# Optimization experiments

Measured on AMD Instinct MI355X. Metric: run time of the kernel, lower is better.

Reference implementation:

```python
import jax, jax.numpy as jnp
import numpy as np

B, N = 2, 2048
DIM, NH, DH = 640, 10, 64
DINNER = 2560
L = 4
DEMB = 32
NTOKS = [128, 64]
NFEAT = 19
FDIM = 280
FEATD = DIM - DEMB * len(NTOKS)  # 576
SQRTD = float(np.sqrt(DH))


def _ln(x, g, b, eps=1e-5):
    m = jnp.mean(x, -1, keepdims=True)
    v = jnp.var(x, -1, keepdims=True)
    return (x - m) * jax.lax.rsqrt(v + eps) * g + b


def setup_inputs() -> dict:
    key = jax.random.key(0)
    ks = iter(jax.random.split(key, 32))
    s = 0.05
    return {
        "x_feats": jax.random.normal(next(ks), (B, N, NFEAT), jnp.float32),
        "x_toks": jax.random.randint(next(ks), (B, N, 2), 0, 64),
        "mask": jnp.ones((B, N), jnp.float32),
        "emb0": jax.random.normal(next(ks), (NTOKS[0] + 1, DEMB)) * s,
        "emb1": jax.random.normal(next(ks), (NTOKS[1] + 1, DEMB)) * s,
        "feat_w": jax.random.normal(next(ks), (FEATD, NFEAT)) * s,
        "feat_b": jnp.zeros((FEATD,)),
        "qkv_w": jax.random.normal(next(ks), (L, 3 * DIM, DIM)) * s,
        "qkv_b": jnp.zeros((L, 3 * DIM)),
        "o_w": jax.random.normal(next(ks), (L, DIM, DIM)) * s,
        "ln1_g": jnp.ones((L, DIM)), "ln1_b": jnp.zeros((L, DIM)),
        "ln2_g": jnp.ones((L, DIM)), "ln2_b": jnp.zeros((L, DIM)),
        "p1_w": jax.random.normal(next(ks), (L, DINNER, DIM)) * s,
        "p1_b": jnp.zeros((L, DINNER)),
        "p2_w": jax.random.normal(next(ks), (L, DIM, DINNER)) * s,
        "p2_b": jnp.zeros((L, DIM)),
        "fn_g": jnp.ones((DIM,)), "fn_b": jnp.zeros((DIM,)),
        "lin1_w": jax.random.normal(next(ks), (FDIM, DIM)) * s,
        "lin1_b": jnp.zeros((FDIM,)),
        "rb1_w": jax.random.normal(next(ks), (FDIM, FDIM)) * s,
        "rb1_b": jnp.zeros((FDIM,)),
        "rb2_w": jax.random.normal(next(ks), (FDIM, FDIM)) * s,
        "rb2_b": jnp.zeros((FDIM,)),
        "out_w": jax.random.normal(next(ks), (1, FDIM)) * s,
        "out_b": jnp.zeros((1,)),
    }


def _forward(x_feats, x_toks, mask, emb0, emb1, feat_w, feat_b,
             qkv_w, qkv_b, o_w, ln1_g, ln1_b, ln2_g, ln2_b,
             p1_w, p1_b, p2_w, p2_b, fn_g, fn_b,
             lin1_w, lin1_b, rb1_w, rb1_b, rb2_w, rb2_b, out_w, out_b):
    # mask outer product [B,N,N]; additive mask 0 where allowed, -1e20 elsewhere
    mask2 = jnp.einsum('bi,bj->bij', mask, mask)
    add_mask = jnp.where(mask2 > 0, 0.0, -1e20)

    # embeddings + feature projection -> [B,N,DIM]
    Z = jnp.concatenate([emb0[x_toks[..., 0]], emb1[x_toks[..., 1]],
                         x_feats @ feat_w.T + feat_b], axis=-1)

    def layer(Z, prm):
        qw, qb, ow, g1, b1, g2, b2, w1, c1, w2, c2 = prm
        inp = Z
        Zn = _ln(Z, g1, b1)
        # qkv reshaped to [B,N,H,3*DH], chunked along last dim: V, Q, K
        qkv = (Zn @ qw.T + qb).reshape(B, N, NH, 3 * DH)
        V, Q, K = qkv[..., :DH], qkv[..., DH:2 * DH], qkv[..., 2 * DH:]
        W = jnp.einsum('bnhd,bmhd->bhnm', Q, K) / SQRTD + add_mask[:, None]
        W = jax.nn.softmax(W, axis=3) * mask2[:, None]  # post-softmax mult mask
        attn = jnp.einsum('bhnm,bmhd->bnhd', W, V).reshape(B, N, DIM)
        Z = jax.nn.leaky_relu(attn) @ ow.T + inp  # leaky_relu BEFORE o_net
        inp = Z
        Zn = _ln(Z, g2, b2)
        Z = jax.nn.relu(Zn @ w1.T + c1) @ w2.T + c2 + inp
        return Z, None

    Z, _ = jax.lax.scan(layer, Z,
                        (qkv_w, qkv_b, o_w, ln1_g, ln1_b, ln2_g, ln2_b,
                         p1_w, p1_b, p2_w, p2_b))
    Z = _ln(Z, fn_g, fn_b)
    # ranking head: 1x1 convs == per-token linears
    h = Z @ lin1_w.T + lin1_b
    h = h + (jax.nn.relu(h @ rb1_w.T + rb1_b) @ rb2_w.T + rb2_b)
    return (h @ out_w.T + out_b)[..., 0]  # [B,N]


def reference(x_feats, x_toks, mask, emb0, emb1, feat_w, feat_b,
              qkv_w, qkv_b, o_w, ln1_g, ln1_b, ln2_g, ln2_b,
              p1_w, p1_b, p2_w, p2_b, fn_g, fn_b,
              lin1_w, lin1_b, rb1_w, rb1_b, rb2_w, rb2_b, out_w, out_b):
    return _forward(x_feats, x_toks, mask, emb0, emb1, feat_w, feat_b,
                    qkv_w, qkv_b, o_w, ln1_g, ln1_b, ln2_g, ln2_b,
                    p1_w, p1_b, p2_w, p2_b, fn_g, fn_b,
                    lin1_w, lin1_b, rb1_w, rb1_b, rb2_w, rb2_b, out_w, out_b)
```

## Files before the change

kernel.cpp:

```cpp
#include <hip/hip_runtime.h>

#define B_ 2
#define N_ 2048
#define DIM_ 640
#define NH_ 10
#define DH_ 64
#define DINNER_ 2560
#define L_ 4
#define FDIM_ 280
#define FDIMP_ 320
#define FEATD_ 576
#define NFEAT_ 19
#define ROWS_ (B_*N_)
#define NSPLIT_ 4
#define NT2_ 16

typedef __attribute__((ext_vector_type(8))) unsigned short ushort8;
typedef __attribute__((ext_vector_type(4))) unsigned short ushort4v;
typedef __attribute__((ext_vector_type(4))) unsigned int u32x4;
typedef __attribute__((ext_vector_type(8))) __bf16 bf16x8;
typedef __attribute__((ext_vector_type(4))) __bf16 bf16x4;
typedef __attribute__((ext_vector_type(4))) float f32x4;
typedef __attribute__((ext_vector_type(2))) unsigned int u32x2;

static __device__ __forceinline__ unsigned short f2bf(float f){
  unsigned int u = __builtin_bit_cast(unsigned int, f);
  u += 0x7fffu + ((u >> 16) & 1u);
  return (unsigned short)(u >> 16);
}

static __device__ __forceinline__ void cvt4(const float* __restrict__ s, unsigned short* __restrict__ d){
  f32x4 v = *(const f32x4*)s;
  ushort4v r;
  r[0]=f2bf(v[0]); r[1]=f2bf(v[1]); r[2]=f2bf(v[2]); r[3]=f2bf(v[3]);
  *(ushort4v*)d = r;
}

static __device__ __forceinline__ f32x4 mfma16(ushort8 a, ushort8 b, f32x4 c){
  return __builtin_amdgcn_mfma_f32_16x16x32_bf16(
      __builtin_bit_cast(bf16x8, a), __builtin_bit_cast(bf16x8, b), c, 0, 0, 0);
}

#define GLD(src,dst) __builtin_amdgcn_global_load_lds((const __attribute__((address_space(1))) void*)(src), (__attribute__((address_space(3))) void*)(dst), 16, 0, 0)

#define SEG0 4915200
#define SEG1 1638400
#define SEG2 6553600
#define SEG3 6553600
#define SEG4 179200
#define SEG5 89600
#define SEG6 89600
#define SEG7 655360
#define SEG8 655360
#define SEG9 4096
#define E0 SEG0
#define E9 (SEG0+SEG1+SEG2+SEG3+SEG4+SEG5+SEG6+SEG7+SEG8+SEG9)

__global__ __launch_bounds__(256) void prep_kernel(
    const float* __restrict__ qkv_w, const float* __restrict__ o_w,
    const float* __restrict__ p1_w, const float* __restrict__ p2_w,
    const float* __restrict__ lin1_w, const float* __restrict__ rb1_w,
    const float* __restrict__ rb2_w, const float* __restrict__ mask,
    unsigned short* __restrict__ qkvw, unsigned short* __restrict__ oww,
    unsigned short* __restrict__ p1w, unsigned short* __restrict__ p2w,
    unsigned short* __restrict__ l1w, unsigned short* __restrict__ r1w,
    unsigned short* __restrict__ r2w, unsigned int* __restrict__ hb1z,
    unsigned int* __restrict__ hb2z, float* __restrict__ mbb)
{
  for (int i = blockIdx.x*256 + threadIdx.x; i < E9/4; i += gridDim.x*256){
    int j = i*4;
    if (j < E0) { cvt4(qkv_w+j, qkvw+j); continue; }
    j -= E0;
    if (j < SEG1) { cvt4(o_w+j, oww+j); continue; }
    j -= SEG1;
    if (j < SEG2) { cvt4(p1_w+j, p1w+j); continue; }
    j -= SEG2;
    if (j < SEG3) { cvt4(p2_w+j, p2w+j); continue; }
    j -= SEG3;
    if (j < SEG4) { cvt4(lin1_w+j, l1w+j); continue; }
    j -= SEG4;
    if (j < SEG5) {
      #pragma unroll
      for (int e=0;e<4;e++){ int jj=j+e; int r=jj/FDIMP_, c=jj-r*FDIMP_;
        r1w[jj] = (c<FDIM_) ? f2bf(rb1_w[r*FDIM_+c]) : (unsigned short)0; }
      continue; }
    j -= SEG5;
    if (j < SEG6) {
      #pragma unroll
      for (int e=0;e<4;e++){ int jj=j+e; int r=jj/FDIMP_, c=jj-r*FDIMP_;
        r2w[jj] = (c<FDIM_) ? f2bf(rb2_w[r*FDIM_+c]) : (unsigned short)0; }
      continue; }
    j -= SEG6;
    if (j < SEG7) { *(u32x4*)(hb1z+j) = u32x4{0u,0u,0u,0u}; continue; }
    j -= SEG7;
    if (j < SEG8) { *(u32x4*)(hb2z+j) = u32x4{0u,0u,0u,0u}; continue; }
    j -= SEG8;
    {
      f32x4 m = *(const f32x4*)(mask+j);
      f32x4 r;
      #pragma unroll
      for (int e=0;e<4;e++) r[e] = (m[e] > 0.f) ? 0.f : -1e30f;
      *(f32x4*)(mbb+j) = r;
    }
  }
}

__global__ __launch_bounds__(256) void embed_kernel(const float* __restrict__ xf,
    const int* __restrict__ xt, const float* __restrict__ e0, const float* __restrict__ e1,
    const float* __restrict__ fw, const float* __restrict__ fb, float* __restrict__ Z){
  int row = blockIdx.x;
  __shared__ float f[NFEAT_];
  int t = threadIdx.x;
  if (t < NFEAT_) f[t] = xf[row*NFEAT_ + t];
  __syncthreads();
  if (t < 32) {
    int tok0 = xt[row*2];
    Z[(size_t)row*DIM_ + t] = e0[tok0*32 + t];
  } else if (t < 64) {
    int tok1 = xt[row*2+1];
    Z[(size_t)row*DIM_ + t] = e1[tok1*32 + (t-32)];
  }
  for (int fo = t; fo < FEATD_; fo += 256){
    float acc = fb[fo];
    #pragma unroll
    for (int k=0;k<NFEAT_;k++) acc += f[k]*fw[fo*NFEAT_+k];
    Z[(size_t)row*DIM_ + 64 + fo] = acc;
  }
}

__global__ __launch_bounds__(256) void ln_kernel(const float* __restrict__ X,
    const float* __restrict__ g, const float* __restrict__ bb,
    unsigned short* __restrict__ out){
  int lane = threadIdx.x & 63;
  int row = blockIdx.x*4 + (threadIdx.x >> 6);
  const float* x = X + (size_t)row*DIM_;
  float v[10]; float s=0.f, sq=0.f;
  #pragma unroll
  for (int j=0;j<10;j++){ float t = x[lane + j*64]; v[j]=t; s+=t; sq+=t*t; }
  #pragma unroll
  for (int off=1; off<64; off<<=1){ s += __shfl_xor(s, off, 64); sq += __shfl_xor(sq, off, 64); }
  float mean = s*(1.f/DIM_);
  float var = sq*(1.f/DIM_) - mean*mean;
  float rstd = rsqrtf(var + 1e-5f);
  unsigned short* o = out + (size_t)row*DIM_;
  #pragma unroll
  for (int j=0;j<10;j++){ int c = lane + j*64; o[c] = f2bf((v[j]-mean)*rstd*g[c] + bb[c]); }
}

template<bool BIAS, bool RELU, bool RES, bool OUTF, bool OUTB>
__global__ __launch_bounds__(256) void gemm_kernel(
    const unsigned short* __restrict__ A, int lda,
    const unsigned short* __restrict__ Bw, int ldb,
    const float* __restrict__ bias,
    const float* __restrict__ Res, int ldres,
    float* __restrict__ Cf, int ldcf,
    unsigned short* __restrict__ Cb, int ldcb,
    int Ncols, int K)
{
  __shared__ __align__(128) unsigned short As[2][8192];
  __shared__ __align__(128) unsigned short Bs[2][8192];
  int t = threadIdx.x;
  int wid = t >> 6, lane = t & 63;
  int wr = wid >> 1, wc = wid & 1;
  int lg = lane >> 4, lm = lane & 15;
  int orig = blockIdx.y*gridDim.x + blockIdx.x;
  int nwg = gridDim.x*gridDim.y;
  int wg = ((orig & 7) * (nwg >> 3)) + (orig >> 3);
  int bx = wg % gridDim.x, by = wg / gridDim.x;
  int row0 = by * 128;
  int col0 = bx * 128;

  const unsigned short* aSrc[4];
  const unsigned short* bSrc[4];
  #pragma unroll
  for (int j=0;j<4;j++){
    int s = t + j*256;
    int r = s >> 3;
    int c = (s & 7) ^ (((r >> 2) & 1) << 1);
    aSrc[j] = A + (size_t)(row0 + r)*lda + c*8;
    int br = col0 + r; if (br >= Ncols) br = Ncols - 1;
    bSrc[j] = Bw + (size_t)br*ldb + c*8;
  }

  f32x4 acc[4][4];
  #pragma unroll
  for (int m=0;m<4;m++)
    #pragma unroll
    for (int n=0;n<4;n++) acc[m][n] = f32x4{0.f,0.f,0.f,0.f};

  int nk = K >> 6;
  #pragma unroll
  for (int j=0;j<4;j++){
    GLD(aSrc[j], &As[0][(t + j*256)*8]);
    GLD(bSrc[j], &Bs[0][(t + j*256)*8]);
  }

  int swz = (lm & 4) >> 1;
  for (int tk=0; tk<nk; ++tk){
    int cur = tk & 1;
    if (tk+1 < nk){
      int kt = (tk+1) << 6;
      #pragma unroll
      for (int j=0;j<4;j++){
        GLD(aSrc[j]+kt, &As[cur^1][(t + j*256)*8]);
        GLD(bSrc[j]+kt, &Bs[cur^1][(t + j*256)*8]);
      }
      asm volatile("s_waitcnt vmcnt(8)" ::: "memory");
    } else {
      asm volatile("s_waitcnt vmcnt(0)" ::: "memory");
    }
    __builtin_amdgcn_s_barrier();
    asm volatile("" ::: "memory");
    const unsigned short* Ac = &As[cur][0];
    const unsigned short* Bc = &Bs[cur][0];
    #pragma unroll
    for (int kk=0;kk<2;kk++){
      int ch = ((kk*4 + lg) ^ swz) * 8;
      ushort8 af[4], bfr[4];
      #pragma unroll
      for (int m=0;m<4;m++) af[m] = *(const ushort8*)(Ac + (wr*64 + m*16 + lm)*64 + ch);
      #pragma unroll
      for (int n=0;n<4;n++) bfr[n] = *(const ushort8*)(Bc + (wc*64 + n*16 + lm)*64 + ch);
      #pragma unroll
      for (int m=0;m<4;m++)
        #pragma unroll
        for (int n=0;n<4;n++)
          acc[m][n] = mfma16(af[m], bfr[n], acc[m][n]);
    }
    asm volatile("" ::: "memory");
    __builtin_amdgcn_s_barrier();
  }

  #pragma unroll
  for (int m=0;m<4;m++){
    int rbase = row0 + wr*64 + m*16 + lg*4;
    #pragma unroll
    for (int n=0;n<4;n++){
      int cc = col0 + wc*64 + n*16 + lm;
      if (cc < Ncols){
        float bv = 0.f;
        if (BIAS) bv = bias[cc];
        #pragma unroll
        for (int rr=0;rr<4;rr++){
          float v = acc[m][n][rr] + bv;
          if (RELU) v = fmaxf(v, 0.f);
          if (RES) v += Res[(size_t)(rbase+rr)*ldres + cc];
          if (OUTF) Cf[(size_t)(rbase+rr)*ldcf + cc] = v;
          if (OUTB) Cb[(size_t)(rbase+rr)*ldcb + cc] = f2bf(v);
        }
      }
    }
  }
}

template<bool BIAS, bool RELU, bool RES, bool OUTF, bool OUTB>
__global__ __launch_bounds__(256) void gemm64_kernel(
    const unsigned short* __restrict__ A, int lda,
    const unsigned short* __restrict__ Bw, int ldb,
    const float* __restrict__ bias,
    const float* __restrict__ Res, int ldres,
    float* __restrict__ Cf, int ldcf,
    unsigned short* __restrict__ Cb, int ldcb,
    int Ncols, int K)
{
  __shared__ __align__(128) unsigned short As[2][64*64];
  __shared__ __align__(128) unsigned short Bs[2][64*64];
  int t = threadIdx.x;
  int wid = t >> 6, lane = t & 63;
  int wr = wid >> 1, wc = wid & 1;
  int lg = lane >> 4, lm = lane & 15;
  int orig = blockIdx.y*gridDim.x + blockIdx.x;
  int nwg = gridDim.x*gridDim.y;
  int wg = ((orig & 7) * (nwg >> 3)) + (orig >> 3);
  int bx = wg % gridDim.x, by = wg / gridDim.x;
  int row0 = by * 64;
  int col0 = bx * 64;

  int ar0 = t >> 3;
  int ar1 = ar0 + 32;
  int aq = (t & 7) ^ (((ar0 >> 2) & 1) << 1);
  const unsigned short* a0 = A + (size_t)(row0+ar0)*lda + aq*8;
  const unsigned short* a1 = A + (size_t)(row0+ar1)*lda + aq*8;
  int br0 = col0+ar0; if (br0 >= Ncols) br0 = Ncols-1;
  int br1 = col0+ar1; if (br1 >= Ncols) br1 = Ncols-1;
  const unsigned short* b0 = Bw + (size_t)br0*ldb + aq*8;
  const unsigned short* b1 = Bw + (size_t)br1*ldb + aq*8;
  int l0 = t*8, l1 = (t+256)*8;

  f32x4 acc[2][2];
  #pragma unroll
  for (int m=0;m<2;m++)
    #pragma unroll
    for (int n=0;n<2;n++) acc[m][n] = f32x4{0.f,0.f,0.f,0.f};

  int nk = K >> 6;
  GLD(a0, &As[0][l0]); GLD(b0, &Bs[0][l0]);
  GLD(a1, &As[0][l1]); GLD(b1, &Bs[0][l1]);

  int swz = (lm & 4) >> 1;
  for (int tk=0; tk<nk; ++tk){
    int cur = tk & 1;
    if (tk+1 < nk){
      int koff = (tk+1) << 6;
      GLD(a0+koff, &As[cur^1][l0]); GLD(b0+koff, &Bs[cur^1][l0]);
      GLD(a1+koff, &As[cur^1][l1]); GLD(b1+koff, &Bs[cur^1][l1]);
      asm volatile("s_waitcnt vmcnt(4)" ::: "memory");
    } else {
      asm volatile("s_waitcnt vmcnt(0)" ::: "memory");
    }
    __builtin_amdgcn_s_barrier();
    asm volatile("" ::: "memory");
    const unsigned short* Ac = &As[cur][0];
    const unsigned short* Bc = &Bs[cur][0];
    #pragma unroll
    for (int kk=0;kk<2;kk++){
      int ch = ((kk*4 + lg) ^ swz) * 8;
      ushort8 af[2], bfr[2];
      #pragma unroll
      for (int m=0;m<2;m++) af[m] = *(const ushort8*)(Ac + (wr*32 + m*16 + lm)*64 + ch);
      #pragma unroll
      for (int n=0;n<2;n++) bfr[n] = *(const ushort8*)(Bc + (wc*32 + n*16 + lm)*64 + ch);
      #pragma unroll
      for (int m=0;m<2;m++)
        #pragma unroll
        for (int n=0;n<2;n++)
          acc[m][n] = mfma16(af[m], bfr[n], acc[m][n]);
    }
    asm volatile("" ::: "memory");
    __builtin_amdgcn_s_barrier();
  }

  #pragma unroll
  for (int m=0;m<2;m++){
    int rbase = row0 + wr*32 + m*16 + lg*4;
    #pragma unroll
    for (int n=0;n<2;n++){
      int cc = col0 + wc*32 + n*16 + lm;
      if (cc < Ncols){
        float bv = 0.f;
        if (BIAS) bv = bias[cc];
        #pragma unroll
        for (int rr=0;rr<4;rr++){
          float v = acc[m][n][rr] + bv;
          if (RELU) v = fmaxf(v, 0.f);
          if (RES) v += Res[(size_t)(rbase+rr)*ldres + cc];
          if (OUTF) Cf[(size_t)(rbase+rr)*ldcf + cc] = v;
          if (OUTB) Cb[(size_t)(rbase+rr)*ldcb + cc] = f2bf(v);
        }
      }
    }
  }
}

__global__ __launch_bounds__(256) void attn_kernel(const unsigned short* __restrict__ qkv,
    const float* __restrict__ mb, unsigned short* __restrict__ op, float* __restrict__ lpp){
  int bh = blockIdx.y; int b = bh/NH_, h = bh%NH_;
  int t = threadIdx.x; int wid = t>>6, lane = t&63, lg = lane>>4, lm = lane&15;
  int q0 = blockIdx.x*64 + wid*16;
  int k0 = blockIdx.z * (NT2_*32);
  size_t prow = (size_t)blockIdx.z*ROWS_ + b*N_;

  __shared__ __align__(128) unsigned short Ks[2][2048];
  __shared__ __align__(128) unsigned short Vs[2][2048];
  __shared__ __align__(16) float maskL[NT2_*32];

  const size_t base = (size_t)b*N_*1920 + (size_t)h*192;
  const size_t kvoff = (size_t)k0*1920;

  int kk0 = t>>3, kc0 = (t&7)^(kk0&7);
  const unsigned short* kS0 = qkv + base + kvoff + 128 + (size_t)kk0*1920 + kc0*8;
  int vk0 = ((t>>5)<<2)|((t>>1)&3), vd0 = (((t>>3)&3)<<1)|(t&1);
  const unsigned short* vS0 = qkv + base + kvoff + (size_t)vk0*1920 + vd0*8;

  ushort8 qf[2];
  #pragma unroll
  for (int ss=0; ss<2; ss++)
    qf[ss] = *(const ushort8*)(qkv + base + (size_t)(q0+lm)*1920 + 64 + ss*32 + lg*8);
  float cb2 = mb[b*N_ + q0 + lm] - 17.3123405f;

  if (t < 128) GLD(mb + b*N_ + k0 + t*4, &maskL[t*4]);
  GLD(kS0, &Ks[0][t*8]);
  GLD(vS0, &Vs[0][t*8]);

  float lp = 0.f;
  f32x4 o[4];
  #pragma unroll
  for (int dn=0;dn<4;dn++) o[dn] = f32x4{0.f,0.f,0.f,0.f};

  for (int ii=0; ii<NT2_; ++ii){
    int cur = ii & 1;
    if (ii < NT2_ - 1){
      const size_t adv = (size_t)(ii+1)*32*1920;
      GLD(kS0+adv, &Ks[1-cur][t*8]);
      GLD(vS0+adv, &Vs[1-cur][t*8]);
      asm volatile("s_waitcnt vmcnt(2)" ::: "memory");
    } else {
      asm volatile("s_waitcnt vmcnt(0)" ::: "memory");
    }
    __builtin_amdgcn_s_barrier();
    asm volatile("" ::: "memory");

    const unsigned short* Kc = &Ks[cur][0];
    f32x4 sf[2];
    #pragma unroll
    for (int c=0;c<2;c++){
      int krow = c*16 + lm;
      f32x4 s = f32x4{0.f,0.f,0.f,0.f};
      #pragma unroll
      for (int ss=0;ss<2;ss++){
        ushort8 kf = *(const ushort8*)(Kc + (krow*8 + ((ss*4+lg)^(krow&7)))*8);
        s = mfma16(kf, qf[ss], s);
      }
      sf[c] = s;
    }
    f32x4 mkv[2];
    #pragma unroll
    for (int c=0;c<2;c++) mkv[c] = *(const f32x4*)&maskL[ii*32 + c*16 + lg*4];

    unsigned vsb = (unsigned)(size_t)(__attribute__((address_space(3))) unsigned short*)&Vs[cur][0];
    unsigned a0 = vsb + lg*512 + lm*8;
    u32x2 vb[2][4];
    asm volatile(
      "ds_read_b64_tr_b16 %0, %4 offset:0\n\t"
      "ds_read_b64_tr_b16 %1, %4 offset:128\n\t"
      "ds_read_b64_tr_b16 %2, %4 offset:256\n\t"
      "ds_read_b64_tr_b16 %3, %4 offset:384"
      : "=&v"(vb[0][0]),"=&v"(vb[0][1]),"=&v"(vb[0][2]),"=&v"(vb[0][3]) : "v"(a0));
    asm volatile(
      "ds_read_b64_tr_b16 %0, %4 offset:2048\n\t"
      "ds_read_b64_tr_b16 %1, %4 offset:2176\n\t"
      "ds_read_b64_tr_b16 %2, %4 offset:2304\n\t"
      "ds_read_b64_tr_b16 %3, %4 offset:2432"
      : "=&v"(vb[1][0]),"=&v"(vb[1][1]),"=&v"(vb[1][2]),"=&v"(vb[1][3]) : "v"(a0));

    float pm[2][4]; bf16x4 pa[2];
    #pragma unroll
    for (int c=0;c<2;c++){
      #pragma unroll
      for (int r=0;r<4;r++){
        float x = fmaf(sf[c][r], 0.18033688f, cb2 + mkv[c][r]);
        pm[c][r] = __builtin_amdgcn_exp2f(x);
      }
      lp += (pm[c][0]+pm[c][1]) + (pm[c][2]+pm[c][3]);
      pa[c] = bf16x4{(__bf16)pm[c][0], (__bf16)pm[c][1], (__bf16)pm[c][2], (__bf16)pm[c][3]};
    }

#define PVM(dn_, c_) asm("v_mfma_f32_16x16x16_bf16 %0, %1, %2, %0" \
      : "+v"(o[dn_]) : "v"(__builtin_bit_cast(u32x2, pa[c_])), "v"(vb[c_][dn_]))
    asm volatile("s_waitcnt lgkmcnt(4)" ::: "memory");
    __builtin_amdgcn_sched_barrier(0);
    __builtin_amdgcn_s_setprio(1);
    PVM(0,0); PVM(1,0); PVM(2,0); PVM(3,0);
    asm volatile("s_waitcnt lgkmcnt(0)" ::: "memory");
    __builtin_amdgcn_sched_barrier(0);
    PVM(0,1); PVM(1,1); PVM(2,1); PVM(3,1);
    __builtin_amdgcn_s_setprio(0);
#undef PVM
    asm volatile("" ::: "memory");
    __builtin_amdgcn_s_barrier();
  }

  float s = lp;
  s += __shfl_xor(s, 16, 64);
  s += __shfl_xor(s, 32, 64);
  if (lg == 0) lpp[(prow + q0 + lm)*NH_ + h] = s;
  #pragma unroll
  for (int r=0;r<4;r++){
    unsigned short* ob = op + (prow + q0 + lg*4 + r)*DIM_ + h*64;
    #pragma unroll
    for (int dn=0;dn<4;dn++)
      ob[dn*16 + lm] = f2bf(o[dn][r]);
  }
}

__global__ __launch_bounds__(256) void attnred_kernel(const unsigned short* __restrict__ op,
    const float* __restrict__ lpp, unsigned short* __restrict__ att){
  int idx = blockIdx.x*256 + threadIdx.x;
  int row = idx / 80;
  int c8 = (idx - row*80) * 8;
  int h = c8 >> 6;
  float l = 0.f;
  #pragma unroll
  for (int s=0;s<NSPLIT_;s++) l += lpp[((size_t)s*ROWS_ + row)*NH_ + h];
  float inv = 1.0f / fmaxf(l, 1e-30f);
  float acc[8] = {0.f,0.f,0.f,0.f,0.f,0.f,0.f,0.f};
  #pragma unroll
  for (int s=0;s<NSPLIT_;s++){
    ushort8 v = *(const ushort8*)(op + ((size_t)s*ROWS_ + row)*DIM_ + c8);
    #pragma unroll
    for (int j=0;j<8;j++) acc[j] += __builtin_bit_cast(float, (unsigned)v[j] << 16);
  }
  ushort8 rr;
  #pragma unroll
  for (int j=0;j<8;j++){
    float v = acc[j] * inv;
    v = (v >= 0.f) ? v : 0.01f*v;
    rr[j] = f2bf(v);
  }
  *(ushort8*)(att + (size_t)row*DIM_ + c8) = rr;
}

__global__ __launch_bounds__(256) void out_kernel(const float* __restrict__ hf,
    const float* __restrict__ ow, const float* __restrict__ ob, float* __restrict__ out){
  int lane = threadIdx.x & 63;
  int row = blockIdx.x*4 + (threadIdx.x>>6);
  const float* x = hf + (size_t)row*FDIM_;
  float s = 0.f;
  for (int j=lane;j<FDIM_;j+=64) s += x[j]*ow[j];
  #pragma unroll
  for (int off=1; off<64; off<<=1) s += __shfl_xor(s, off, 64);
  if (lane==0) out[row] = s + ob[0];
}

extern "C" void kernel_launch(void* const* d_in, const int* in_sizes, int n_in,
                              void* d_out, int out_size, void* d_ws, size_t ws_size,
                              hipStream_t stream)
{
  const float* x_feats = (const float*)d_in[0];
  const int*   x_toks  = (const int*)d_in[1];
  const float* mask    = (const float*)d_in[2];
  const float* emb0    = (const float*)d_in[3];
  const float* emb1    = (const float*)d_in[4];
  const float* feat_w  = (const float*)d_in[5];
  const float* feat_b  = (const float*)d_in[6];
  const float* qkv_w   = (const float*)d_in[7];
  const float* qkv_b   = (const float*)d_in[8];
  const float* o_w     = (const float*)d_in[9];
  const float* ln1_g   = (const float*)d_in[10];
  const float* ln1_b   = (const float*)d_in[11];
  const float* ln2_g   = (const float*)d_in[12];
  const float* ln2_b   = (const float*)d_in[13];
  const float* p1_w    = (const float*)d_in[14];
  const float* p1_b    = (const float*)d_in[15];
  const float* p2_w    = (const float*)d_in[16];
  const float* p2_b    = (const float*)d_in[17];
  const float* fn_g    = (const float*)d_in[18];
  const float* fn_b    = (const float*)d_in[19];
  const float* lin1_w  = (const float*)d_in[20];
  const float* lin1_b  = (const float*)d_in[21];
  const float* rb1_w   = (const float*)d_in[22];
  const float* rb1_b   = (const float*)d_in[23];
  const float* rb2_w   = (const float*)d_in[24];
  const float* rb2_b   = (const float*)d_in[25];
  const float* out_w   = (const float*)d_in[26];
  const float* out_b   = (const float*)d_in[27];
  float* out = (float*)d_out;

  char* w = (char*)d_ws;
  auto alloc = [&](size_t bytes)->void*{ void* p = (void*)w; w += (bytes + 255) & ~(size_t)255; return p; };

  float* Z              = (float*)alloc((size_t)ROWS_*DIM_*4);
  unsigned short* Zn    = (unsigned short*)alloc((size_t)ROWS_*DIM_*2);
  unsigned short* qkvB  = (unsigned short*)alloc((size_t)ROWS_*1920*2);
  unsigned short* attB  = (unsigned short*)alloc((size_t)ROWS_*DIM_*2);
  unsigned short* Hb    = (unsigned short*)alloc((size_t)ROWS_*DINNER_*2);
  float* hf             = (float*)alloc((size_t)ROWS_*FDIM_*4);
  unsigned short* hb1   = (unsigned short*)alloc((size_t)ROWS_*FDIMP_*2);
  unsigned short* hb2   = (unsigned short*)alloc((size_t)ROWS_*FDIMP_*2);
  float* mbb            = (float*)alloc((size_t)ROWS_*4);
  unsigned short* opart = (unsigned short*)alloc((size_t)NSPLIT_*ROWS_*DIM_*2);
  float* lpart          = (float*)alloc((size_t)NSPLIT_*ROWS_*NH_*4);
  unsigned short* qkvw  = (unsigned short*)alloc((size_t)L_*1920*DIM_*2);
  unsigned short* oww   = (unsigned short*)alloc((size_t)L_*DIM_*DIM_*2);
  unsigned short* p1w   = (unsigned short*)alloc((size_t)L_*DINNER_*DIM_*2);
  unsigned short* p2w   = (unsigned short*)alloc((size_t)L_*DIM_*DINNER_*2);
  unsigned short* l1w   = (unsigned short*)alloc((size_t)FDIM_*DIM_*2);
  unsigned short* r1w   = (unsigned short*)alloc((size_t)FDIM_*FDIMP_*2);
  unsigned short* r2w   = (unsigned short*)alloc((size_t)FDIM_*FDIMP_*2);

  prep_kernel<<<2048,256,0,stream>>>(qkv_w, o_w, p1_w, p2_w, lin1_w, rb1_w, rb2_w, mask,
      qkvw, oww, p1w, p2w, l1w, r1w, r2w,
      (unsigned int*)hb1, (unsigned int*)hb2, mbb);

  embed_kernel<<<ROWS_,256,0,stream>>>(x_feats, x_toks, emb0, emb1, feat_w, feat_b, Z);

  for (int l=0; l<L_; l++){
    ln_kernel<<<ROWS_/4,256,0,stream>>>(Z, ln1_g + l*DIM_, ln1_b + l*DIM_, Zn);
    gemm_kernel<true,false,false,false,true><<<dim3(15,32),256,0,stream>>>(
        Zn, DIM_, qkvw + (size_t)l*1920*DIM_, DIM_, qkv_b + l*1920,
        nullptr, 0, nullptr, 0, qkvB, 1920, 1920, DIM_);
    attn_kernel<<<dim3(N_/64, B_*NH_, NSPLIT_),256,0,stream>>>(qkvB, mbb, opart, lpart);
    attnred_kernel<<<ROWS_*80/256,256,0,stream>>>(opart, lpart, attB);
    gemm64_kernel<false,false,true,true,false><<<dim3(10,64),256,0,stream>>>(
        attB, DIM_, oww + (size_t)l*DIM_*DIM_, DIM_, nullptr,
        Z, DIM_, Z, DIM_, nullptr, 0, DIM_, DIM_);
    ln_kernel<<<ROWS_/4,256,0,stream>>>(Z, ln2_g + l*DIM_, ln2_b + l*DIM_, Zn);
    gemm_kernel<true,true,false,false,true><<<dim3(20,32),256,0,stream>>>(
        Zn, DIM_, p1w + (size_t)l*DINNER_*DIM_, DIM_, p1_b + l*DINNER_,
        nullptr, 0, nullptr, 0, Hb, DINNER_, DINNER_, DIM_);
    gemm64_kernel<true,false,true,true,false><<<dim3(10,64),256,0,stream>>>(
        Hb, DINNER_, p2w + (size_t)l*DIM_*DINNER_, DINNER_, p2_b + l*DIM_,
        Z, DIM_, Z, DIM_, nullptr, 0, DIM_, DINNER_);
  }

  ln_kernel<<<ROWS_/4,256,0,stream>>>(Z, fn_g, fn_b, Zn);
  gemm64_kernel<true,false,false,true,true><<<dim3(5,64),256,0,stream>>>(
      Zn, DIM_, l1w, DIM_, lin1_b, nullptr, 0, hf, FDIM_, hb1, FDIMP_, FDIM_, DIM_);
  gemm64_kernel<true,true,false,false,true><<<dim3(5,64),256,0,stream>>>(
      hb1, FDIMP_, r1w, FDIMP_, rb1_b, nullptr, 0, nullptr, 0, hb2, FDIMP_, FDIM_, FDIMP_);
  gemm64_kernel<true,false,true,true,false><<<dim3(5,64),256,0,stream>>>(
      hb2, FDIMP_, r2w, FDIMP_, rb2_b, hf, FDIM_, hf, FDIM_, nullptr, 0, FDIM_, FDIMP_);
  out_kernel<<<ROWS_/4,256,0,stream>>>(hf, out_w, out_b, out);
}
```

Baseline: 639.5 us.

## Process two 16-row query tiles per wave in attention to reuse K/V loads

```diff
diff --git a/kernel.cpp b/kernel.cpp
--- a/kernel.cpp
+++ b/kernel.cpp
@@ -356,7 +356,7 @@
     const float* __restrict__ mb, unsigned short* __restrict__ op, float* __restrict__ lpp){
   int bh = blockIdx.y; int b = bh/NH_, h = bh%NH_;
   int t = threadIdx.x; int wid = t>>6, lane = t&63, lg = lane>>4, lm = lane&15;
-  int q0 = blockIdx.x*64 + wid*16;
+  int q0 = blockIdx.x*128 + wid*32;
   int k0 = blockIdx.z * (NT2_*32);
   size_t prow = (size_t)blockIdx.z*ROWS_ + b*N_;
 
@@ -372,20 +372,23 @@
   int vk0 = ((t>>5)<<2)|((t>>1)&3), vd0 = (((t>>3)&3)<<1)|(t&1);
   const unsigned short* vS0 = qkv + base + kvoff + (size_t)vk0*1920 + vd0*8;
 
-  ushort8 qf[2];
-  #pragma unroll
-  for (int ss=0; ss<2; ss++)
-    qf[ss] = *(const ushort8*)(qkv + base + (size_t)(q0+lm)*1920 + 64 + ss*32 + lg*8);
-  float cb2 = mb[b*N_ + q0 + lm] - 17.3123405f;
+  ushort8 qfA[2], qfB[2];
+  #pragma unroll
+  for (int ss=0; ss<2; ss++){
+    qfA[ss] = *(const ushort8*)(qkv + base + (size_t)(q0+lm)*1920 + 64 + ss*32 + lg*8);
+    qfB[ss] = *(const ushort8*)(qkv + base + (size_t)(q0+16+lm)*1920 + 64 + ss*32 + lg*8);
+  }
+  float cb2A = mb[b*N_ + q0 + lm] - 17.3123405f;
+  float cb2B = mb[b*N_ + q0 + 16 + lm] - 17.3123405f;
 
   if (t < 128) GLD(mb + b*N_ + k0 + t*4, &maskL[t*4]);
   GLD(kS0, &Ks[0][t*8]);
   GLD(vS0, &Vs[0][t*8]);
 
-  float lp = 0.f;
-  f32x4 o[4];
-  #pragma unroll
-  for (int dn=0;dn<4;dn++) o[dn] = f32x4{0.f,0.f,0.f,0.f};
+  float lpA = 0.f, lpB = 0.f;
+  f32x4 oA[4], oB[4];
+  #pragma unroll
+  for (int dn=0;dn<4;dn++){ oA[dn] = f32x4{0.f,0.f,0.f,0.f}; oB[dn] = f32x4{0.f,0.f,0.f,0.f}; }
 
   for (int ii=0; ii<NT2_; ++ii){
     int cur = ii & 1;
@@ -401,17 +404,19 @@
     asm volatile("" ::: "memory");
 
     const unsigned short* Kc = &Ks[cur][0];
-    f32x4 sf[2];
+    f32x4 sfA[2], sfB[2];
     #pragma unroll
     for (int c=0;c<2;c++){
       int krow = c*16 + lm;
-      f32x4 s = f32x4{0.f,0.f,0.f,0.f};
+      f32x4 sA = f32x4{0.f,0.f,0.f,0.f};
+      f32x4 sB = f32x4{0.f,0.f,0.f,0.f};
       #pragma unroll
       for (int ss=0;ss<2;ss++){
         ushort8 kf = *(const ushort8*)(Kc + (krow*8 + ((ss*4+lg)^(krow&7)))*8);
-        s = mfma16(kf, qf[ss], s);
+        sA = mfma16(kf, qfA[ss], sA);
+        sB = mfma16(kf, qfB[ss], sB);
       }
-      sf[c] = s;
+      sfA[c] = sA; sfB[c] = sB;
     }
     f32x4 mkv[2];
     #pragma unroll
@@ -433,43 +438,54 @@
       "ds_read_b64_tr_b16 %3, %4 offset:2432"
       : "=&v"(vb[1][0]),"=&v"(vb[1][1]),"=&v"(vb[1][2]),"=&v"(vb[1][3]) : "v"(a0));
 
-    float pm[2][4]; bf16x4 pa[2];
+    bf16x4 paA[2], paB[2];
     #pragma unroll
     for (int c=0;c<2;c++){
+      float pm[4], pn[4];
       #pragma unroll
       for (int r=0;r<4;r++){
-        float x = fmaf(sf[c][r], 0.18033688f, cb2 + mkv[c][r]);
-        pm[c][r] = __builtin_amdgcn_exp2f(x);
+        pm[r] = __builtin_amdgcn_exp2f(fmaf(sfA[c][r], 0.18033688f, cb2A + mkv[c][r]));
+        pn[r] = __builtin_amdgcn_exp2f(fmaf(sfB[c][r], 0.18033688f, cb2B + mkv[c][r]));
       }
-      lp += (pm[c][0]+pm[c][1]) + (pm[c][2]+pm[c][3]);
-      pa[c] = bf16x4{(__bf16)pm[c][0], (__bf16)pm[c][1], (__bf16)pm[c][2], (__bf16)pm[c][3]};
-    }
-
-#define PVM(dn_, c_) asm("v_mfma_f32_16x16x16_bf16 %0, %1, %2, %0" \
-      : "+v"(o[dn_]) : "v"(__builtin_bit_cast(u32x2, pa[c_])), "v"(vb[c_][dn_]))
+      lpA += (pm[0]+pm[1]) + (pm[2]+pm[3]);
+      lpB += (pn[0]+pn[1]) + (pn[2]+pn[3]);
+      paA[c] = bf16x4{(__bf16)pm[0], (__bf16)pm[1], (__bf16)pm[2], (__bf16)pm[3]};
+      paB[c] = bf16x4{(__bf16)pn[0], (__bf16)pn[1], (__bf16)pn[2], (__bf16)pn[3]};
+    }
+
+#define PVM(o_, p_, v_) asm("v_mfma_f32_16x16x16_bf16 %0, %1, %2, %0" \
+      : "+v"(o_) : "v"(__builtin_bit_cast(u32x2, p_)), "v"(v_))
     asm volatile("s_waitcnt lgkmcnt(4)" ::: "memory");
     __builtin_amdgcn_sched_barrier(0);
     __builtin_amdgcn_s_setprio(1);
-    PVM(0,0); PVM(1,0); PVM(2,0); PVM(3,0);
+    PVM(oA[0],paA[0],vb[0][0]); PVM(oA[1],paA[0],vb[0][1]); PVM(oA[2],paA[0],vb[0][2]); PVM(oA[3],paA[0],vb[0][3]);
+    PVM(oB[0],paB[0],vb[0][0]); PVM(oB[1],paB[0],vb[0][1]); PVM(oB[2],paB[0],vb[0][2]); PVM(oB[3],paB[0],vb[0][3]);
     asm volatile("s_waitcnt lgkmcnt(0)" ::: "memory");
     __builtin_amdgcn_sched_barrier(0);
-    PVM(0,1); PVM(1,1); PVM(2,1); PVM(3,1);
+    PVM(oA[0],paA[1],vb[1][0]); PVM(oA[1],paA[1],vb[1][1]); PVM(oA[2],paA[1],vb[1][2]); PVM(oA[3],paA[1],vb[1][3]);
+    PVM(oB[0],paB[1],vb[1][0]); PVM(oB[1],paB[1],vb[1][1]); PVM(oB[2],paB[1],vb[1][2]); PVM(oB[3],paB[1],vb[1][3]);
     __builtin_amdgcn_s_setprio(0);
 #undef PVM
     asm volatile("" ::: "memory");
     __builtin_amdgcn_s_barrier();
   }
 
-  float s = lp;
-  s += __shfl_xor(s, 16, 64);
-  s += __shfl_xor(s, 32, 64);
-  if (lg == 0) lpp[(prow + q0 + lm)*NH_ + h] = s;
+  float sA = lpA, sB = lpB;
+  sA += __shfl_xor(sA, 16, 64); sA += __shfl_xor(sA, 32, 64);
+  sB += __shfl_xor(sB, 16, 64); sB += __shfl_xor(sB, 32, 64);
+  if (lg == 0){
+    lpp[(prow + q0 + lm)*NH_ + h] = sA;
+    lpp[(prow + q0 + 16 + lm)*NH_ + h] = sB;
+  }
   #pragma unroll
   for (int r=0;r<4;r++){
-    unsigned short* ob = op + (prow + q0 + lg*4 + r)*DIM_ + h*64;
-    #pragma unroll
-    for (int dn=0;dn<4;dn++)
-      ob[dn*16 + lm] = f2bf(o[dn][r]);
+    unsigned short* obA = op + (prow + q0 + lg*4 + r)*DIM_ + h*64;
+    unsigned short* obB = op + (prow + q0 + 16 + lg*4 + r)*DIM_ + h*64;
+    #pragma unroll
+    for (int dn=0;dn<4;dn++){
+      obA[dn*16 + lm] = f2bf(oA[dn][r]);
+      obB[dn*16 + lm] = f2bf(oB[dn][r]);
+    }
   }
 }
 
@@ -579,7 +595,7 @@
     gemm_kernel<true,false,false,false,true><<<dim3(15,32),256,0,stream>>>(
         Zn, DIM_, qkvw + (size_t)l*1920*DIM_, DIM_, qkv_b + l*1920,
         nullptr, 0, nullptr, 0, qkvB, 1920, 1920, DIM_);
-    attn_kernel<<<dim3(N_/64, B_*NH_, NSPLIT_),256,0,stream>>>(qkvB, mbb, opart, lpart);
+    attn_kernel<<<dim3(N_/128, B_*NH_, NSPLIT_),256,0,stream>>>(qkvB, mbb, opart, lpart);
     attnred_kernel<<<ROWS_*80/256,256,0,stream>>>(opart, lpart, attB);
     gemm64_kernel<false,false,true,true,false><<<dim3(10,64),256,0,stream>>>(
         attB, DIM_, oww + (size_t)l*DIM_*DIM_, DIM_, nullptr,
```

Result: no change. 641.8 us (+0.4%).
